# Kernel tuning notes

Hardware: AMD Instinct MI355X
Metric: run time of the kernel (lower is better)

Reference implementation:

```python
import jax, jax.numpy as jnp
import numpy as np

N, C, K, B, G = 32768, 128, 16, 4, 8
SCALE, BASE = 2.0, 10000.0

def _bn(x, gamma, beta, eps=1e-5):
    # torch BatchNorm1d (training): stats over all axes except channel (last)
    axes = tuple(range(x.ndim - 1))
    mean = x.mean(axes)
    var = x.var(axes)
    return (x - mean) / jnp.sqrt(var + eps) * gamma + beta

def _cayley_rope(x, coord, S_param):
    c = x.shape[-1]
    S = jnp.triu(S_param, 1)
    S = S - S.T
    I = jnp.eye(c, dtype=x.dtype)
    P = jnp.linalg.solve(I + S, I - S)  # (I+S)^-1 (I-S)
    xr = x @ P.T
    dpa = c // 3 // 2 * 2          # dim per axis (even)
    dr = dpa * 3                   # rotated dims
    inv_freq = 1.0 / (BASE ** (jnp.arange(0, dpa, 2, dtype=jnp.float32) / dpa))
    cs = coord * SCALE
    def rot(f, c1):
        ang = c1[:, None] * inv_freq[None, :]
        s, co = jnp.sin(ang), jnp.cos(ang)
        fr, fi = jnp.split(f, 2, axis=-1)
        return jnp.concatenate([fr * co - fi * s, fr * s + fi * co], -1)
    parts = [rot(xr[:, i * dpa:(i + 1) * dpa], cs[:, i]) for i in range(3)]
    out = jnp.concatenate(parts + [xr[:, dr:]], -1)
    return out @ P

def setup_inputs() -> dict:
    key = jax.random.key(0)
    ks = jax.random.split(key, 24)
    w = lambda k, i, o, s=0.02: jax.random.normal(k, (i, o), jnp.float32) * s
    inp = {
        'feat': jax.random.normal(ks[0], (N, C), jnp.float32),
        'coord': jax.random.uniform(ks[1], (N, 3), jnp.float32) * 10.0,
        'reference_index': jax.random.randint(ks[2], (N, K), 0, N),
        'offset': jnp.arange(1, B + 1, dtype=jnp.int32) * (N // B),
        'Wq': w(ks[3], C, C), 'bq': jnp.zeros((C,)),
        'gq': jnp.ones((C,)), 'bnq': jnp.zeros((C,)),
        'Wk': w(ks[4], C, C), 'bk': jnp.zeros((C,)),
        'gk': jnp.ones((C,)), 'bnk': jnp.zeros((C,)),
        'Wv': w(ks[5], C, C), 'bv': jnp.zeros((C,)),
        'S_param': jax.random.normal(ks[6], (C, C), jnp.float32) * 0.01,
        'Ww1': w(ks[7], C, G), 'bw1': jnp.zeros((G,)),
        'gw': jnp.ones((G,)), 'bnw': jnp.zeros((G,)),
        'Ww2': w(ks[8], G, G), 'bw2': jnp.zeros((G,)),
        'Wg1': w(ks[9], 2 * C, C), 'bg1': jnp.zeros((C,)),
        'gg': jnp.ones((C,)), 'bng': jnp.zeros((C,)),
        'Wg2': w(ks[10], C, G, 0.001), 'bg2': jnp.full((G,), 3.0),
    }
    return inp

def reference(feat, coord, reference_index, offset, Wq, bq, gq, bnq, Wk, bk, gk, bnk,
              Wv, bv, S_param, Ww1, bw1, gw, bnw, Ww2, bw2, Wg1, bg1, gg, bng, Wg2, bg2):
    q_raw = jax.nn.relu(_bn(feat @ Wq + bq, gq, bnq))
    k_raw = jax.nn.relu(_bn(feat @ Wk + bk, gk, bnk))
    value = feat @ Wv + bv
    q = _cayley_rope(q_raw, coord, S_param)
    k = _cayley_rope(k_raw, coord, S_param)
    kg = k[reference_index]            # [N,K,C] gather
    vg = value[reference_index]        # [N,K,C]
    rel = kg - q[:, None, :]
    geom = jax.nn.relu(_bn(rel @ Ww1 + bw1, gw, bnw)) @ Ww2 + bw2  # [N,K,G]
    seg = jnp.searchsorted(offset, jnp.arange(N), side='right')
    gmax = jax.ops.segment_max(q_raw, seg, num_segments=B)
    gate_in = jnp.concatenate([q_raw, gmax[seg]], -1)              # [N,2C]
    gate = jax.nn.sigmoid(jax.nn.relu(_bn(gate_in @ Wg1 + bg1, gg, bng)) @ Wg2 + bg2)  # [N,G]
    refined = geom * (1.0 + gate[:, None, :])
    attn = jax.nn.softmax(refined, axis=1)
    mask = jnp.sign(reference_index + 1).astype(attn.dtype)
    attn = attn * mask[:, :, None]
    vg4 = vg.reshape(N, K, G, C // G)
    out = jnp.einsum('nkgi,nkg->ngi', vg4, attn).reshape(N, C)
    return out
```

## Files before the change

### kernel.cpp

```cpp
#include <hip/hip_runtime.h>
#include <math.h>

#define N_PTS 32768
#define C_DIM 128
#define K_NB  16
#define G_DIM 8

#define OF_PW     0
#define OF_STATQ  1024
#define OF_STATK  1280
#define OF_STATG1 1536
#define OF_STATH  1792
#define OF_UMAXP  1808
#define OF_UMAXN  2320
#define OF_WQT    4096
#define OF_WKT    12288
#define OF_WVT    20480
#define OF_WG1T   28672
#define OF_PTMIT  36864
#define OF_QW     65536
#define OF_KW     327680
#define OF_GATE   589824
#define OF_G1     1048576
#define OF_V      5242880

typedef short bf16x8 __attribute__((ext_vector_type(8)));
typedef float f32x4  __attribute__((ext_vector_type(4)));

#define LSTR 136

__device__ __forceinline__ unsigned f2bf(float f) {
  unsigned u = __float_as_uint(f);
  return (u + 0x7fffu + ((u >> 16) & 1u)) >> 16;
}
__device__ __forceinline__ float bf2f(short s) {
  return __uint_as_float(((unsigned)(unsigned short)s) << 16);
}
__device__ __forceinline__ unsigned fenc(float f) {
  unsigned b = __float_as_uint(f);
  return (b & 0x80000000u) ? ~b : (b | 0x80000000u);
}
__device__ __forceinline__ float fdec(unsigned u) {
  unsigned b = (u & 0x80000000u) ? (u & 0x7fffffffu) : ~u;
  return __uint_as_float(b);
}
__device__ __forceinline__ bf16x8 pack_bf8(float4 a, float4 b) {
  bf16x8 r;
  r[0] = (short)f2bf(a.x); r[1] = (short)f2bf(a.y);
  r[2] = (short)f2bf(a.z); r[3] = (short)f2bf(a.w);
  r[4] = (short)f2bf(b.x); r[5] = (short)f2bf(b.y);
  r[6] = (short)f2bf(b.z); r[7] = (short)f2bf(b.w);
  return r;
}
__device__ __forceinline__ float fetch_asym(const float* M, int r, int c) {
  return (c > r) ? M[r*128 + c] : ((c < r) ? -M[c*128 + r] : 0.f);
}

__device__ __forceinline__ void g2l16(const void* g, void* l) {
  __builtin_amdgcn_global_load_lds(
      (const __attribute__((address_space(1))) void*)g,
      (__attribute__((address_space(3))) void*)l, 16, 0, 0);
}

__device__ __forceinline__ void stage_async(short* dst, const short* __restrict__ src, int tid) {
  int lane = tid & 63, wv = tid >> 6;
  #pragma unroll
  for (int it = 0; it < 8; ++it) {
    int chunk = it*256 + wv*64;
    int D = (chunk + lane)*16;
    int gs = D ^ (((D >> 8) & 7) << 4);
    g2l16((const char*)src + gs, (char*)dst + chunk*16);
  }
}

__device__ __forceinline__ f32x4 mfma1(const short* Bb, const bf16x8* a4, int row, int quad) {
  f32x4 ac = {0.f, 0.f, 0.f, 0.f};
  int sx = (row & 7) << 4;
  #pragma unroll
  for (int ks = 0; ks < 4; ++ks) {
    const char* p = (const char*)Bb + (((row*256) + ks*64 + quad*16) ^ sx);
    ac = __builtin_amdgcn_mfma_f32_16x16x32_bf16(a4[ks], *(const bf16x8*)p, ac, 0, 0, 0);
  }
  return ac;
}

__global__ __launch_bounds__(256) void cayley(const float* __restrict__ Sp,
    const float* __restrict__ Ww1,
    const float* __restrict__ Wq, const float* __restrict__ Wk,
    const float* __restrict__ Wv, const float* __restrict__ Wg1,
    short* __restrict__ WqT, short* __restrict__ WkT,
    short* __restrict__ WvT, short* __restrict__ Wg1T,
    short* __restrict__ PTmIT, float* __restrict__ PW,
    float* __restrict__ statz)
{
  __shared__ short Ssh[128*LSTR];
  __shared__ float x0[128], x1[128];
  int bx = blockIdx.x, tid = threadIdx.x;
  if (bx >= 64) {
    if (bx < 80) {
      int idx = bx - 64, widx = idx >> 2, qr = idx & 3;
      const float* src = (widx == 0) ? Wq : (widx == 1) ? Wk : (widx == 2) ? Wv : Wg1;
      short* dst = (widx == 0) ? WqT : (widx == 1) ? WkT : (widx == 2) ? WvT : Wg1T;
      const float4* s4 = (const float4*)src;
      #pragma unroll
      for (int it = 0; it < 4; ++it) {
        int q = it*256 + tid; int k = qr*32 + (q >> 5), n4 = q & 31;
        float4 v = s4[k*32 + n4];
        dst[(n4*4+0)*128 + k] = (short)f2bf(v.x);
        dst[(n4*4+1)*128 + k] = (short)f2bf(v.y);
        dst[(n4*4+2)*128 + k] = (short)f2bf(v.z);
        dst[(n4*4+3)*128 + k] = (short)f2bf(v.w);
      }
    } else {
      #pragma unroll
      for (int it = 0; it < 8; ++it) {
        int idx = it*256 + tid;
        if (idx < 1808) statz[idx] = 0.f;
      }
    }
    return;
  }
  int c0 = bx*2, c1 = c0 + 1;
  #pragma unroll 8
  for (int it = 0; it < 64; ++it) {
    int idx = it*256 + tid; int i = idx >> 7, j = idx & 127;
    Ssh[i*LSTR + j] = (short)f2bf(fetch_asym(Sp, i, j));
  }
  if (tid < 128) {
    x0[tid] = (tid == c0) ? 1.f : 0.f;
    x1[tid] = (tid == c1) ? 1.f : 0.f;
  }
  __syncthreads();
  int i = tid >> 1, h = tid & 1;
  const short* srow = &Ssh[i*LSTR + h*64];
  for (int t = 0; t < 16; ++t) {
    float a0 = 0.f, a1 = 0.f;
    #pragma unroll
    for (int jq = 0; jq < 16; ++jq) {
      short4 sv = *(const short4*)&srow[jq*4];
      #pragma unroll
      for (int u = 0; u < 4; ++u) {
        float s = bf2f((&sv.x)[u]);
        int j = h*64 + jq*4 + u;
        a0 = fmaf(s, x0[j], a0);
        a1 = fmaf(s, x1[j], a1);
      }
    }
    a0 += __shfl_xor(a0, 1);
    a1 += __shfl_xor(a1, 1);
    __syncthreads();
    if (h == 0) {
      x0[i] = a0 + ((i == c0) ? 1.f : 0.f);
      x1[i] = a1 + ((i == c1) ? 1.f : 0.f);
    }
    __syncthreads();
  }
  if (tid < 128) {
    PTmIT[c0*128 + tid] = (short)f2bf(2.f*x0[tid] - ((tid == c0) ? 2.f : 0.f));
  } else {
    int t = tid - 128;
    PTmIT[c1*128 + t] = (short)f2bf(2.f*x1[t] - ((t == c1) ? 2.f : 0.f));
  }
  if (tid < 16) {
    int cc = tid >> 3, g = tid & 7;
    const float* xv = cc ? x1 : x0;
    int c = cc ? c1 : c0;
    float acc = 0.f;
    #pragma unroll 8
    for (int j = 0; j < 128; ++j) acc = fmaf(xv[j], Ww1[j*8 + g], acc);
    PW[c*8 + g] = 2.f*acc - Ww1[c*8 + g];
  }
}

__global__ __launch_bounds__(256, 2) void qkv_mfma(const float* __restrict__ feat,
    const short* __restrict__ WqT, const short* __restrict__ WkT, const short* __restrict__ WvT,
    const float* __restrict__ bq, const float* __restrict__ bk, const float* __restrict__ bv,
    float* __restrict__ Vv,
    float* __restrict__ statq, float* __restrict__ statk,
    unsigned* __restrict__ umaxp, unsigned* __restrict__ umaxn)
{
  __shared__ __align__(16) short Bb0[128*128];
  __shared__ __align__(16) short Bb1[128*128];
  __shared__ float ssum[2][128], ssq[2][128];
  __shared__ unsigned ump[128], umn[128];
  int tid = threadIdx.x, row0 = blockIdx.x * 64, seg = row0 >> 13;
  int lane = tid & 63, w = tid >> 6, l15 = lane & 15, quad = lane >> 4;
  stage_async(Bb0, WqT, tid);
  if (tid < 128) {
    ssum[0][tid] = 0.f; ssum[1][tid] = 0.f;
    ssq[0][tid] = 0.f;  ssq[1][tid] = 0.f;
    ump[tid] = 0u; umn[tid] = 0u;
  }
  bf16x8 af[4];
  {
    long rbase = (long)(row0 + w*16 + l15) * 128;
    #pragma unroll
    for (int ks = 0; ks < 4; ++ks) {
      int c0 = ks*32 + quad*8;
      float4 v0 = *(const float4*)&feat[rbase + c0];
      float4 v1 = *(const float4*)&feat[rbase + c0 + 4];
      af[ks] = pack_bf8(v0, v1);
    }
  }
  __syncthreads();
  stage_async(Bb1, WkT, tid);
  {
    #pragma unroll
    for (int nt = 0; nt < 8; ++nt) {
      f32x4 ac = mfma1(Bb0, af, nt*16 + l15, quad);
      int col = nt*16 + l15;
      float bb = bq[col];
      float s = 0.f, s2 = 0.f, mx = -1e30f, mn = 1e30f;
      #pragma unroll
      for (int r = 0; r < 4; ++r) {
        float raw = ac[r];
        float v = raw + bb;
        s += v; s2 = fmaf(v, v, s2);
        mx = fmaxf(mx, raw); mn = fminf(mn, raw);
      }
      s += __shfl_xor(s, 16); s += __shfl_xor(s, 32);
      s2 += __shfl_xor(s2, 16); s2 += __shfl_xor(s2, 32);
      mx = fmaxf(mx, __shfl_xor(mx, 16)); mx = fmaxf(mx, __shfl_xor(mx, 32));
      mn = fminf(mn, __shfl_xor(mn, 16)); mn = fminf(mn, __shfl_xor(mn, 32));
      if (lane < 16) {
        atomicAdd(&ssum[0][col], s); atomicAdd(&ssq[0][col], s2);
        atomicMax(&ump[col], fenc(mx)); atomicMax(&umn[col], fenc(-mn));
      }
    }
  }
  __syncthreads();
  stage_async(Bb0, WvT, tid);
  {
    #pragma unroll
    for (int nt = 0; nt < 8; ++nt) {
      f32x4 ac = mfma1(Bb1, af, nt*16 + l15, quad);
      int col = nt*16 + l15;
      float bb = bk[col];
      float s = 0.f, s2 = 0.f;
      #pragma unroll
      for (int r = 0; r < 4; ++r) {
        float v = ac[r] + bb;
        s += v; s2 = fmaf(v, v, s2);
      }
      s += __shfl_xor(s, 16); s += __shfl_xor(s, 32);
      s2 += __shfl_xor(s2, 16); s2 += __shfl_xor(s2, 32);
      if (lane < 16) { atomicAdd(&ssum[1][col], s); atomicAdd(&ssq[1][col], s2); }
    }
  }
  __syncthreads();
  {
    #pragma unroll
    for (int nt = 0; nt < 8; ++nt) {
      f32x4 ac = mfma1(Bb0, af, nt*16 + l15, quad);
      int col = nt*16 + l15;
      float bb = bv[col];
      #pragma unroll
      for (int r = 0; r < 4; ++r)
        Vv[(long)(row0 + w*16 + quad*4 + r)*128 + col] = ac[r] + bb;
    }
  }
  __syncthreads();
  if (tid < 128) {
    atomicAdd(&statq[tid], ssum[0][tid]); atomicAdd(&statq[128 + tid], ssq[0][tid]);
    atomicAdd(&statk[tid], ssum[1][tid]); atomicAdd(&statk[128 + tid], ssq[1][tid]);
    atomicMax(&umaxp[seg*128 + tid], ump[tid]);
    atomicMax(&umaxn[seg*128 + tid], umn[tid]);
  }
}

__global__ __launch_bounds__(256) void rqkw(
    const float* __restrict__ feat,
    const short* __restrict__ WqT, const short* __restrict__ WkT,
    const short* __restrict__ PTmIT, const short* __restrict__ Wg1T,
    const float* __restrict__ coord,
    const float* __restrict__ bq, const float* __restrict__ bk,
    const float* __restrict__ statq, const float* __restrict__ statk,
    const float* __restrict__ gq, const float* __restrict__ bnq,
    const float* __restrict__ gk, const float* __restrict__ bnk,
    const unsigned* __restrict__ umaxp, const unsigned* __restrict__ umaxn,
    const float* __restrict__ Wg1, const float* __restrict__ bg1,
    const float* __restrict__ PW, const float* __restrict__ bw1,
    float* __restrict__ qw, float* __restrict__ kw,
    float* __restrict__ g1, float* __restrict__ statg1)
{
  __shared__ __align__(16) char arena[58880];
  __shared__ float caq[128], cbq[128], cak[128], cbk[128];
  __shared__ float gml[128], gsg[128];
  __shared__ float ssum[128], ssq[128];
  short* featS = (short*)arena;
  short* bnqS  = (short*)(arena + 8704);
  short* bnkS  = (short*)(arena + 17408);
  short* Bbuf  = (short*)(arena + 26112);
  float* xsq = (float*)arena;
  float* xsk = (float*)(arena + 16896);
  float* pws = (float*)(arena + 33792);
  int tid = threadIdx.x;
  int row0 = blockIdx.x * 32, seg = row0 >> 13;
  const float invn = 1.f / 32768.f;
  stage_async(Bbuf, WqT, tid);
  if (tid < 128) {
    float m = statq[tid]*invn, vv = fmaf(-m, m, statq[128 + tid]*invn);
    float a = rsqrtf(vv + 1e-5f) * gq[tid];
    float b = fmaf(-m, a, bnq[tid]);
    float cb2 = fmaf(a, bq[tid], b);
    caq[tid] = a; cbq[tid] = cb2;
    float mx = fdec(umaxp[seg*128 + tid]);
    float mn = -fdec(umaxn[seg*128 + tid]);
    gml[tid] = fmaxf(0.f, fmaxf(fmaf(a, mx, cb2), fmaf(a, mn, cb2)));
    m = statk[tid]*invn; vv = fmaf(-m, m, statk[128 + tid]*invn);
    a = rsqrtf(vv + 1e-5f) * gk[tid];
    b = fmaf(-m, a, bnk[tid]);
    cak[tid] = a; cbk[tid] = fmaf(a, bk[tid], b);
    ssum[tid] = 0.f; ssq[tid] = 0.f;
  }
  {
    const float4* s4 = (const float4*)feat;
    #pragma unroll
    for (int it = 0; it < 4; ++it) {
      int q = it*256 + tid; int r = q >> 5, c4 = q & 31;
      float4 v = s4[(long)(row0 + r)*32 + c4];
      uint2 p;
      p.x = f2bf(v.x) | (f2bf(v.y) << 16);
      p.y = f2bf(v.z) | (f2bf(v.w) << 16);
      *(uint2*)&featS[r*LSTR + c4*4] = p;
    }
  }
  __syncthreads();
  int lane = tid & 63, w = tid >> 6, l15 = lane & 15, quad = lane >> 4;
  bool isq = (w < 2);
  int rw = (w & 1) * 16;
  const float* ca = isq ? caq : cak;
  const float* cb = isq ? cbq : cbk;
  bf16x8 af[4];
  #pragma unroll
  for (int ks = 0; ks < 4; ++ks)
    af[ks] = *(bf16x8*)&featS[(rw + l15)*LSTR + ks*32 + quad*8];

  float bnl[32];
  if (isq) {
    #pragma unroll
    for (int nt = 0; nt < 8; ++nt) {
      f32x4 ac = mfma1(Bbuf, af, nt*16 + l15, quad);
      int col = nt*16 + l15;
      float A = ca[col], B = cb[col];
      #pragma unroll
      for (int r = 0; r < 4; ++r) {
        float v = fmaxf(0.f, fmaf(A, ac[r], B));
        bnl[nt*4 + r] = v;
        bnqS[(rw + quad*4 + r)*LSTR + col] = (short)f2bf(v);
      }
    }
  }
  __syncthreads();
  stage_async(Bbuf, WkT, tid);
  __syncthreads();
  if (!isq) {
    #pragma unroll
    for (int nt = 0; nt < 8; ++nt) {
      f32x4 ac = mfma1(Bbuf, af, nt*16 + l15, quad);
      int col = nt*16 + l15;
      float A = ca[col], B = cb[col];
      #pragma unroll
      for (int r = 0; r < 4; ++r) {
        float v = fmaxf(0.f, fmaf(A, ac[r], B));
        bnl[nt*4 + r] = v;
        bnkS[(rw + quad*4 + r)*LSTR + col] = (short)f2bf(v);
      }
    }
  } else if (tid < 128) {
    float acc = bg1[tid];
    #pragma unroll 8
    for (int j = 0; j < 128; ++j)
      acc = fmaf(gml[j], Wg1[(128 + j)*128 + tid], acc);
    gsg[tid] = acc;
  }
  __syncthreads();
  stage_async(Bbuf, PTmIT, tid);
  bf16x8 af2[4];
  {
    const short* bnS = isq ? bnqS : bnkS;
    #pragma unroll
    for (int ks = 0; ks < 4; ++ks)
      af2[ks] = *(bf16x8*)&bnS[(rw + l15)*LSTR + ks*32 + quad*8];
  }
  __syncthreads();
  f32x4 accv[8];
  #pragma unroll
  for (int nt = 0; nt < 8; ++nt)
    accv[nt] = mfma1(Bbuf, af2, nt*16 + l15, quad);
  __syncthreads();
  stage_async(Bbuf, Wg1T, tid);
  __syncthreads();
  f32x4 accw[8];
  if (isq) {
    #pragma unroll
    for (int nt = 0; nt < 8; ++nt)
      accw[nt] = mfma1(Bbuf, af2, nt*16 + l15, quad);
  }
  __syncthreads();
  {
    float* xs = isq ? xsq : xsk;
    #pragma unroll
    for (int nt = 0; nt < 8; ++nt) {
      int col = nt*16 + l15;
      #pragma unroll
      for (int r = 0; r < 4; ++r)
        xs[(rw + quad*4 + r)*132 + col] = accv[nt][r] + bnl[nt*4 + r];
    }
  }
  #pragma unroll
  for (int it = 0; it < 4; ++it) { int idx = tid + it*256; pws[idx] = PW[idx]; }
  if (isq) {
    #pragma unroll
    for (int nt = 0; nt < 8; ++nt) {
      int col = nt*16 + l15;
      float gsv = gsg[col];
      float s = 0.f, s2 = 0.f;
      #pragma unroll
      for (int r = 0; r < 4; ++r) {
        float v = accw[nt][r] + gsv;
        int row = row0 + rw + quad*4 + r;
        g1[(long)row*128 + col] = v;
        s += v; s2 = fmaf(v, v, s2);
      }
      s += __shfl_xor(s, 16); s += __shfl_xor(s, 32);
      s2 += __shfl_xor(s2, 16); s2 += __shfl_xor(s2, 32);
      if (lane < 16) { atomicAdd(&ssum[col], s); atomicAdd(&ssq[col], s2); }
    }
  }
  __syncthreads();
  #pragma unroll
  for (int it = 0; it < 8; ++it) {
    int idx = it*256 + tid;
    int r = idx >> 6, s = idx & 63;
    if (s < 63) {
      int a3 = s / 21, j = s - a3*21;
      int cr = a3*42 + j;
      float invf = exp2f((float)(2*j) * (-13.287712379549449f / 42.f));
      float ang = coord[(row0 + r)*3 + a3] * (2.0f * invf);
      float sn, co; sincosf(ang, &sn, &co);
      float fr = xsq[r*132 + cr], fi = xsq[r*132 + cr + 21];
      xsq[r*132 + cr]      = fr*co - fi*sn;
      xsq[r*132 + cr + 21] = fr*sn + fi*co;
      fr = xsk[r*132 + cr]; fi = xsk[r*132 + cr + 21];
      xsk[r*132 + cr]      = fr*co - fi*sn;
      xsk[r*132 + cr + 21] = fr*sn + fi*co;
    }
  }
  __syncthreads();
  #pragma unroll
  for (int it = 0; it < 2; ++it) {
    int idx = it*256 + tid;
    int mat = idx >> 8, r2 = (idx >> 3) & 31, g = idx & 7;
    const float* x2 = mat ? xsk : xsq;
    float a0 = 0.f, a1 = 0.f, a2 = 0.f, a3 = 0.f;
    #pragma unroll 8
    for (int i = 0; i < 128; i += 4) {
      float4 xv = *(const float4*)&x2[r2*132 + i];
      a0 = fmaf(xv.x, pws[(i+0)*8 + g], a0);
      a1 = fmaf(xv.y, pws[(i+1)*8 + g], a1);
      a2 = fmaf(xv.z, pws[(i+2)*8 + g], a2);
      a3 = fmaf(xv.w, pws[(i+3)*8 + g], a3);
    }
    float acc = (a0 + a1) + (a2 + a3) + (mat ? bw1[g] : 0.f);
    float* dst = mat ? kw : qw;
    dst[(long)(row0 + r2)*8 + g] = acc;
  }
  if (tid < 128) {
    atomicAdd(&statg1[tid], ssum[tid]);
    atomicAdd(&statg1[128 + tid], ssq[tid]);
  }
}

__global__ __launch_bounds__(256) void mid(
    const float* __restrict__ g1, const float* __restrict__ statg1,
    const float* __restrict__ ggm, const float* __restrict__ bng,
    const float* __restrict__ Wg2, const float* __restrict__ bg2,
    float* __restrict__ gate,
    const float* __restrict__ kw, const float* __restrict__ qw,
    const int* __restrict__ ref, float* __restrict__ stath)
{
  __shared__ float gs[32][132];
  __shared__ float w2s[128][8];
  __shared__ float cA[128], cB[128];
  __shared__ float red[256];
  int tid = threadIdx.x;
  if (blockIdx.x < 1024) {
    int row0 = blockIdx.x * 32;
    #pragma unroll
    for (int it = 0; it < 4; ++it) { int idx = tid + it*256; w2s[idx >> 3][idx & 7] = Wg2[idx]; }
    if (tid < 128) {
      const float invn = 1.f / 32768.f;
      float m = statg1[tid]*invn, v = fmaf(-m, m, statg1[128 + tid]*invn);
      float a = rsqrtf(v + 1e-5f) * ggm[tid];
      cA[tid] = a; cB[tid] = fmaf(-m, a, bng[tid]);
    }
    #pragma unroll
    for (int it = 0; it < 4; ++it) {
      int idx = tid + it*256; int r = idx >> 5, cq = idx & 31;
      *(float4*)&gs[r][cq*4] = *(const float4*)&g1[(long)(row0 + r)*128 + cq*4];
    }
    __syncthreads();
    int r = tid >> 3, g = tid & 7;
    float acc = bg2[g];
    #pragma unroll 8
    for (int c2 = 0; c2 < 128; ++c2) {
      float act = fmaxf(0.f, fmaf(gs[r][c2], cA[c2], cB[c2]));
      acc = fmaf(act, w2s[c2][g], acc);
    }
    gate[(long)(row0 + r)*8 + g] = 1.f / (1.f + expf(-acc));
  } else {
    long base = (long)(blockIdx.x - 1024) * 4096;
    float s = 0.f, sq = 0.f;
    for (int it = 0; it < 16; ++it) {
      long idx = base + it*256 + tid;
      int n = (int)(idx >> 7); int kk = (int)((idx >> 3) & 15); int g = (int)(idx & 7);
      int r = ref[n*16 + kk];
      float h = kw[(long)r*8 + g] - qw[(long)n*8 + g];
      s += h; sq = fmaf(h, h, sq);
    }
    red[tid] = s; __syncthreads();
    for (int d = 128; d >= 8; d >>= 1) { if (tid < d) red[tid] += red[tid + d]; __syncthreads(); }
    if (tid < 8) atomicAdd(&stath[tid], red[tid]);
    __syncthreads();
    red[tid] = sq; __syncthreads();
    for (int d = 128; d >= 8; d >>= 1) { if (tid < d) red[tid] += red[tid + d]; __syncthreads(); }
    if (tid < 8) atomicAdd(&stath[8 + tid], red[tid]);
  }
}

__global__ __launch_bounds__(256) void attn_out(const float* __restrict__ qw, const float* __restrict__ kw,
                                                const float* __restrict__ stath,
                                                const float* __restrict__ gw, const float* __restrict__ bnw,
                                                const float* __restrict__ Ww2, const float* __restrict__ bw2,
                                                const float* __restrict__ gate, const int* __restrict__ ref,
                                                const float* __restrict__ v, float* __restrict__ out)
{
  __shared__ float sm1[2][16][9];
  __shared__ float sm2[2][16][9];
  __shared__ int   smr[2][16];
  int tid = threadIdx.x; int rh = tid >> 7, t = tid & 127;
  int n = blockIdx.x * 2 + rh;
  int kk = t >> 3, g = t & 7;
  if (t < 16) smr[rh][t] = ref[n*16 + t];
  __syncthreads();
  const float invnk = 1.f / 524288.f;
  float m0 = stath[g]*invnk, v0 = fmaf(-m0, m0, stath[8 + g]*invnk);
  float aw = rsqrtf(v0 + 1e-5f) * gw[g];
  float bw = fmaf(-m0, aw, bnw[g]);
  int rr = smr[rh][kk];
  float h = kw[(long)rr*8 + g] - qw[(long)n*8 + g];
  sm1[rh][kk][g] = fmaxf(0.f, fmaf(h, aw, bw));
  __syncthreads();
  float acc = bw2[g];
  #pragma unroll
  for (int g2 = 0; g2 < 8; ++g2) acc = fmaf(sm1[rh][kk][g2], Ww2[g2*8 + g], acc);
  float refined = acc * (1.f + gate[(long)n*8 + g]);
  sm2[rh][kk][g] = refined;
  __syncthreads();
  float mx = -1e30f;
  #pragma unroll
  for (int k2 = 0; k2 < 16; ++k2) mx = fmaxf(mx, sm2[rh][k2][g]);
  float e = expf(refined - mx);
  sm1[rh][kk][g] = e;
  __syncthreads();
  float ssum = 0.f;
  #pragma unroll
  for (int k2 = 0; k2 < 16; ++k2) ssum += sm1[rh][k2][g];
  float mask = ((rr + 1) > 0) ? 1.f : (((rr + 1) == 0) ? 0.f : -1.f);
  float attn = e / ssum * mask;
  sm2[rh][kk][g] = attn;
  __syncthreads();
  float o = 0.f;
  #pragma unroll
  for (int k2 = 0; k2 < 16; ++k2) {
    o = fmaf(v[(long)smr[rh][k2]*128 + t], sm2[rh][k2][t >> 4], o);
  }
  out[(long)n*128 + t] = o;
}

extern "C" void kernel_launch(void* const* d_in, const int* in_sizes, int n_in,
                              void* d_out, int out_size, void* d_ws, size_t ws_size,
                              hipStream_t stream)
{
  const float* feat  = (const float*)d_in[0];
  const float* coord = (const float*)d_in[1];
  const int*   ref   = (const int*)d_in[2];
  const float* Wq  = (const float*)d_in[4];
  const float* bq  = (const float*)d_in[5];
  const float* gq  = (const float*)d_in[6];
  const float* bnq = (const float*)d_in[7];
  const float* Wk  = (const float*)d_in[8];
  const float* bk  = (const float*)d_in[9];
  const float* gk  = (const float*)d_in[10];
  const float* bnk = (const float*)d_in[11];
  const float* Wv  = (const float*)d_in[12];
  const float* bv  = (const float*)d_in[13];
  const float* Sp  = (const float*)d_in[14];
  const float* Ww1 = (const float*)d_in[15];
  const float* bw1 = (const float*)d_in[16];
  const float* gw  = (const float*)d_in[17];
  const float* bnw = (const float*)d_in[18];
  const float* Ww2 = (const float*)d_in[19];
  const float* bw2 = (const float*)d_in[20];
  const float* Wg1 = (const float*)d_in[21];
  const float* bg1 = (const float*)d_in[22];
  const float* ggm = (const float*)d_in[23];
  const float* bng = (const float*)d_in[24];
  const float* Wg2 = (const float*)d_in[25];
  const float* bg2 = (const float*)d_in[26];
  float* out = (float*)d_out;

  float* W = (float*)d_ws;
  float* PW = W + OF_PW;
  short* WqT   = (short*)(W + OF_WQT);
  short* WkT   = (short*)(W + OF_WKT);
  short* WvT   = (short*)(W + OF_WVT);
  short* Wg1T  = (short*)(W + OF_WG1T);
  short* PTmIT = (short*)(W + OF_PTMIT);
  float* G1 = W + OF_G1;
  float* Vv = W + OF_V;

  cayley<<<81, 256, 0, stream>>>(Sp, Ww1, Wq, Wk, Wv, Wg1,
                                 WqT, WkT, WvT, Wg1T, PTmIT, PW, W + OF_STATQ);
  qkv_mfma<<<512, 256, 0, stream>>>(feat, WqT, WkT, WvT, bq, bk, bv, Vv,
                                    W + OF_STATQ, W + OF_STATK,
                                    (unsigned*)(W + OF_UMAXP), (unsigned*)(W + OF_UMAXN));
  rqkw<<<1024, 256, 0, stream>>>(feat, WqT, WkT, PTmIT, Wg1T, coord,
                                 bq, bk,
                                 W + OF_STATQ, W + OF_STATK,
                                 gq, bnq, gk, bnk,
                                 (const unsigned*)(W + OF_UMAXP), (const unsigned*)(W + OF_UMAXN),
                                 Wg1, bg1, PW, bw1,
                                 W + OF_QW, W + OF_KW, G1, W + OF_STATG1);
  mid<<<2048, 256, 0, stream>>>(G1, W + OF_STATG1, ggm, bng, Wg2, bg2, W + OF_GATE,
                                W + OF_KW, W + OF_QW, ref, W + OF_STATH);
  attn_out<<<16384, 256, 0, stream>>>(W + OF_QW, W + OF_KW, W + OF_STATH, gw, bnw, Ww2, bw2,
                                      W + OF_GATE, ref, Vv, out);
}
```

Before: 316.9 us.

## Split rqkw into separate q and k blocks to cut LDS and raise occupancy

```diff
diff --git a/kernel.cpp b/kernel.cpp
--- a/kernel.cpp
+++ b/kernel.cpp
@@ -268,7 +268,7 @@
   }
 }
 
-__global__ __launch_bounds__(256) void rqkw(
+__global__ __launch_bounds__(256, 3) void rqkw(
     const float* __restrict__ feat,
     const short* __restrict__ WqT, const short* __restrict__ WkT,
     const short* __restrict__ PTmIT, const short* __restrict__ Wg1T,
@@ -283,150 +283,116 @@
     float* __restrict__ qw, float* __restrict__ kw,
     float* __restrict__ g1, float* __restrict__ statg1)
 {
-  __shared__ __align__(16) char arena[58880];
-  __shared__ float caq[128], cbq[128], cak[128], cbk[128];
-  __shared__ float gml[128], gsg[128];
-  __shared__ float ssum[128], ssq[128];
-  short* featS = (short*)arena;
-  short* bnqS  = (short*)(arena + 8704);
-  short* bnkS  = (short*)(arena + 17408);
-  short* Bbuf  = (short*)(arena + 26112);
-  float* xsq = (float*)arena;
-  float* xsk = (float*)(arena + 16896);
-  float* pws = (float*)(arena + 33792);
-  int tid = threadIdx.x;
-  int row0 = blockIdx.x * 32, seg = row0 >> 13;
+  __shared__ __align__(16) char arena[41472];
+  __shared__ float ca[128], cb[128];
+  __shared__ float gml[128], gsg[128], ssum[128], ssq[128];
+  short* Bbuf = (short*)arena;
+  short* bnS  = (short*)(arena + 32768);
+  float* xs   = (float*)arena;
+  float* pws  = (float*)(arena + 16896);
+  int tid = threadIdx.x, bx = blockIdx.x;
+  bool isq = (bx & 1) == 0;
+  int row0 = (bx >> 1) * 32, seg = row0 >> 13;
+  int lane = tid & 63, w = tid >> 6, l15 = lane & 15, quad = lane >> 4;
+  int mrow = (w & 1) * 16;
+  int nt0  = (w >> 1) * 4;
+  stage_async(Bbuf, isq ? WqT : WkT, tid);
+  bf16x8 af[4];
+  {
+    long rbase = (long)(row0 + mrow + l15) * 128;
+    #pragma unroll
+    for (int ks = 0; ks < 4; ++ks) {
+      int c0 = ks*32 + quad*8;
+      float4 v0 = *(const float4*)&feat[rbase + c0];
+      float4 v1 = *(const float4*)&feat[rbase + c0 + 4];
+      af[ks] = pack_bf8(v0, v1);
+    }
+  }
   const float invn = 1.f / 32768.f;
-  stage_async(Bbuf, WqT, tid);
   if (tid < 128) {
-    float m = statq[tid]*invn, vv = fmaf(-m, m, statq[128 + tid]*invn);
-    float a = rsqrtf(vv + 1e-5f) * gq[tid];
-    float b = fmaf(-m, a, bnq[tid]);
-    float cb2 = fmaf(a, bq[tid], b);
-    caq[tid] = a; cbq[tid] = cb2;
-    float mx = fdec(umaxp[seg*128 + tid]);
-    float mn = -fdec(umaxn[seg*128 + tid]);
-    gml[tid] = fmaxf(0.f, fmaxf(fmaf(a, mx, cb2), fmaf(a, mn, cb2)));
-    m = statk[tid]*invn; vv = fmaf(-m, m, statk[128 + tid]*invn);
-    a = rsqrtf(vv + 1e-5f) * gk[tid];
-    b = fmaf(-m, a, bnk[tid]);
-    cak[tid] = a; cbk[tid] = fmaf(a, bk[tid], b);
-    ssum[tid] = 0.f; ssq[tid] = 0.f;
-  }
-  {
-    const float4* s4 = (const float4*)feat;
-    #pragma unroll
-    for (int it = 0; it < 4; ++it) {
-      int q = it*256 + tid; int r = q >> 5, c4 = q & 31;
-      float4 v = s4[(long)(row0 + r)*32 + c4];
-      uint2 p;
-      p.x = f2bf(v.x) | (f2bf(v.y) << 16);
-      p.y = f2bf(v.z) | (f2bf(v.w) << 16);
-      *(uint2*)&featS[r*LSTR + c4*4] = p;
-    }
-  }
-  __syncthreads();
-  int lane = tid & 63, w = tid >> 6, l15 = lane & 15, quad = lane >> 4;
-  bool isq = (w < 2);
-  int rw = (w & 1) * 16;
-  const float* ca = isq ? caq : cak;
-  const float* cb = isq ? cbq : cbk;
-  bf16x8 af[4];
-  #pragma unroll
-  for (int ks = 0; ks < 4; ++ks)
-    af[ks] = *(bf16x8*)&featS[(rw + l15)*LSTR + ks*32 + quad*8];
-
-  float bnl[32];
-  if (isq) {
-    #pragma unroll
-    for (int nt = 0; nt < 8; ++nt) {
-      f32x4 ac = mfma1(Bbuf, af, nt*16 + l15, quad);
-      int col = nt*16 + l15;
-      float A = ca[col], B = cb[col];
-      #pragma unroll
-      for (int r = 0; r < 4; ++r) {
-        float v = fmaxf(0.f, fmaf(A, ac[r], B));
-        bnl[nt*4 + r] = v;
-        bnqS[(rw + quad*4 + r)*LSTR + col] = (short)f2bf(v);
-      }
-    }
-  }
-  __syncthreads();
-  stage_async(Bbuf, WkT, tid);
-  __syncthreads();
-  if (!isq) {
-    #pragma unroll
-    for (int nt = 0; nt < 8; ++nt) {
-      f32x4 ac = mfma1(Bbuf, af, nt*16 + l15, quad);
-      int col = nt*16 + l15;
-      float A = ca[col], B = cb[col];
-      #pragma unroll
-      for (int r = 0; r < 4; ++r) {
-        float v = fmaxf(0.f, fmaf(A, ac[r], B));
-        bnl[nt*4 + r] = v;
-        bnkS[(rw + quad*4 + r)*LSTR + col] = (short)f2bf(v);
-      }
-    }
-  } else if (tid < 128) {
+    if (isq) {
+      float m = statq[tid]*invn, vv = fmaf(-m, m, statq[128 + tid]*invn);
+      float a = rsqrtf(vv + 1e-5f) * gq[tid];
+      float b = fmaf(-m, a, bnq[tid]);
+      float cb2 = fmaf(a, bq[tid], b);
+      ca[tid] = a; cb[tid] = cb2;
+      float mx = fdec(umaxp[seg*128 + tid]);
+      float mn = -fdec(umaxn[seg*128 + tid]);
+      gml[tid] = fmaxf(0.f, fmaxf(fmaf(a, mx, cb2), fmaf(a, mn, cb2)));
+      ssum[tid] = 0.f; ssq[tid] = 0.f;
+    } else {
+      float m = statk[tid]*invn, vv = fmaf(-m, m, statk[128 + tid]*invn);
+      float a = rsqrtf(vv + 1e-5f) * gk[tid];
+      float b = fmaf(-m, a, bnk[tid]);
+      ca[tid] = a; cb[tid] = fmaf(a, bk[tid], b);
+    }
+  }
+  __syncthreads();
+  float bnl[16];
+  #pragma unroll
+  for (int nt = 0; nt < 4; ++nt) {
+    f32x4 ac = mfma1(Bbuf, af, (nt0 + nt)*16 + l15, quad);
+    int col = (nt0 + nt)*16 + l15;
+    float A = ca[col], B = cb[col];
+    #pragma unroll
+    for (int r = 0; r < 4; ++r) {
+      float v = fmaxf(0.f, fmaf(A, ac[r], B));
+      bnl[nt*4 + r] = v;
+      bnS[(mrow + quad*4 + r)*LSTR + col] = (short)f2bf(v);
+    }
+  }
+  __syncthreads();
+  stage_async(Bbuf, PTmIT, tid);
+  if (isq && tid < 128) {
     float acc = bg1[tid];
     #pragma unroll 8
     for (int j = 0; j < 128; ++j)
       acc = fmaf(gml[j], Wg1[(128 + j)*128 + tid], acc);
     gsg[tid] = acc;
   }
-  __syncthreads();
-  stage_async(Bbuf, PTmIT, tid);
   bf16x8 af2[4];
-  {
-    const short* bnS = isq ? bnqS : bnkS;
-    #pragma unroll
-    for (int ks = 0; ks < 4; ++ks)
-      af2[ks] = *(bf16x8*)&bnS[(rw + l15)*LSTR + ks*32 + quad*8];
-  }
-  __syncthreads();
-  f32x4 accv[8];
-  #pragma unroll
-  for (int nt = 0; nt < 8; ++nt)
-    accv[nt] = mfma1(Bbuf, af2, nt*16 + l15, quad);
-  __syncthreads();
-  stage_async(Bbuf, Wg1T, tid);
-  __syncthreads();
-  f32x4 accw[8];
+  #pragma unroll
+  for (int ks = 0; ks < 4; ++ks)
+    af2[ks] = *(bf16x8*)&bnS[(mrow + l15)*LSTR + ks*32 + quad*8];
+  __syncthreads();
+  f32x4 accv[4];
+  #pragma unroll
+  for (int nt = 0; nt < 4; ++nt)
+    accv[nt] = mfma1(Bbuf, af2, (nt0 + nt)*16 + l15, quad);
+  __syncthreads();
   if (isq) {
-    #pragma unroll
-    for (int nt = 0; nt < 8; ++nt)
-      accw[nt] = mfma1(Bbuf, af2, nt*16 + l15, quad);
-  }
-  __syncthreads();
-  {
-    float* xs = isq ? xsq : xsk;
-    #pragma unroll
-    for (int nt = 0; nt < 8; ++nt) {
-      int col = nt*16 + l15;
-      #pragma unroll
-      for (int r = 0; r < 4; ++r)
-        xs[(rw + quad*4 + r)*132 + col] = accv[nt][r] + bnl[nt*4 + r];
-    }
-  }
-  #pragma unroll
-  for (int it = 0; it < 4; ++it) { int idx = tid + it*256; pws[idx] = PW[idx]; }
-  if (isq) {
-    #pragma unroll
-    for (int nt = 0; nt < 8; ++nt) {
-      int col = nt*16 + l15;
+    stage_async(Bbuf, Wg1T, tid);
+    __syncthreads();
+    #pragma unroll
+    for (int nt = 0; nt < 4; ++nt) {
+      f32x4 ac = mfma1(Bbuf, af2, (nt0 + nt)*16 + l15, quad);
+      int col = (nt0 + nt)*16 + l15;
       float gsv = gsg[col];
       float s = 0.f, s2 = 0.f;
       #pragma unroll
       for (int r = 0; r < 4; ++r) {
-        float v = accw[nt][r] + gsv;
-        int row = row0 + rw + quad*4 + r;
-        g1[(long)row*128 + col] = v;
+        float v = ac[r] + gsv;
+        g1[(long)(row0 + mrow + quad*4 + r)*128 + col] = v;
         s += v; s2 = fmaf(v, v, s2);
       }
       s += __shfl_xor(s, 16); s += __shfl_xor(s, 32);
       s2 += __shfl_xor(s2, 16); s2 += __shfl_xor(s2, 32);
       if (lane < 16) { atomicAdd(&ssum[col], s); atomicAdd(&ssq[col], s2); }
     }
+    __syncthreads();
+  }
+  #pragma unroll
+  for (int nt = 0; nt < 4; ++nt) {
+    int col = (nt0 + nt)*16 + l15;
+    #pragma unroll
+    for (int r = 0; r < 4; ++r)
+      xs[(mrow + quad*4 + r)*132 + col] = accv[nt][r] + bnl[nt*4 + r];
+  }
+  #pragma unroll
+  for (int it = 0; it < 4; ++it) { int idx = tid + it*256; pws[idx] = PW[idx]; }
+  if (isq && tid < 128) {
+    atomicAdd(&statg1[tid], ssum[tid]);
+    atomicAdd(&statg1[128 + tid], ssq[tid]);
   }
   __syncthreads();
   #pragma unroll
@@ -439,36 +405,26 @@
       float invf = exp2f((float)(2*j) * (-13.287712379549449f / 42.f));
       float ang = coord[(row0 + r)*3 + a3] * (2.0f * invf);
       float sn, co; sincosf(ang, &sn, &co);
-      float fr = xsq[r*132 + cr], fi = xsq[r*132 + cr + 21];
-      xsq[r*132 + cr]      = fr*co - fi*sn;
-      xsq[r*132 + cr + 21] = fr*sn + fi*co;
-      fr = xsk[r*132 + cr]; fi = xsk[r*132 + cr + 21];
-      xsk[r*132 + cr]      = fr*co - fi*sn;
-      xsk[r*132 + cr + 21] = fr*sn + fi*co;
-    }
-  }
-  __syncthreads();
-  #pragma unroll
-  for (int it = 0; it < 2; ++it) {
-    int idx = it*256 + tid;
-    int mat = idx >> 8, r2 = (idx >> 3) & 31, g = idx & 7;
-    const float* x2 = mat ? xsk : xsq;
+      float fr = xs[r*132 + cr], fi = xs[r*132 + cr + 21];
+      xs[r*132 + cr]      = fr*co - fi*sn;
+      xs[r*132 + cr + 21] = fr*sn + fi*co;
+    }
+  }
+  __syncthreads();
+  {
+    int r2 = tid >> 3, g = tid & 7;
     float a0 = 0.f, a1 = 0.f, a2 = 0.f, a3 = 0.f;
     #pragma unroll 8
     for (int i = 0; i < 128; i += 4) {
-      float4 xv = *(const float4*)&x2[r2*132 + i];
+      float4 xv = *(const float4*)&xs[r2*132 + i];
       a0 = fmaf(xv.x, pws[(i+0)*8 + g], a0);
       a1 = fmaf(xv.y, pws[(i+1)*8 + g], a1);
       a2 = fmaf(xv.z, pws[(i+2)*8 + g], a2);
       a3 = fmaf(xv.w, pws[(i+3)*8 + g], a3);
     }
-    float acc = (a0 + a1) + (a2 + a3) + (mat ? bw1[g] : 0.f);
-    float* dst = mat ? kw : qw;
+    float acc = (a0 + a1) + (a2 + a3) + (isq ? 0.f : bw1[g]);
+    float* dst = isq ? qw : kw;
     dst[(long)(row0 + r2)*8 + g] = acc;
-  }
-  if (tid < 128) {
-    atomicAdd(&statg1[tid], ssum[tid]);
-    atomicAdd(&statg1[128 + tid], ssq[tid]);
   }
 }
 
@@ -626,7 +582,7 @@
   qkv_mfma<<<512, 256, 0, stream>>>(feat, WqT, WkT, WvT, bq, bk, bv, Vv,
                                     W + OF_STATQ, W + OF_STATK,
                                     (unsigned*)(W + OF_UMAXP), (unsigned*)(W + OF_UMAXN));
-  rqkw<<<1024, 256, 0, stream>>>(feat, WqT, WkT, PTmIT, Wg1T, coord,
+  rqkw<<<2048, 256, 0, stream>>>(feat, WqT, WkT, PTmIT, Wg1T, coord,
                                  bq, bk,
                                  W + OF_STATQ, W + OF_STATK,
                                  gq, bnq, gk, bnk,
```

After: 321.9 us. No clear change (+1.6%).

## Double-buffer weight staging in rqkw and hoist gate-max projection into a prep kernel

Applied to the files above, without the earlier changes.

```diff
diff --git a/kernel.cpp b/kernel.cpp
--- a/kernel.cpp
+++ b/kernel.cpp
@@ -13,6 +13,7 @@
 #define OF_STATH  1792
 #define OF_UMAXP  1808
 #define OF_UMAXN  2320
+#define OF_GSG    2832
 #define OF_WQT    4096
 #define OF_WKT    12288
 #define OF_WVT    20480
@@ -268,7 +269,35 @@
   }
 }
 
-__global__ __launch_bounds__(256) void rqkw(
+__global__ __launch_bounds__(128) void gprep(
+    const float* __restrict__ statq,
+    const float* __restrict__ gq, const float* __restrict__ bnq,
+    const float* __restrict__ bq,
+    const unsigned* __restrict__ umaxp, const unsigned* __restrict__ umaxn,
+    const float* __restrict__ Wg1, const float* __restrict__ bg1,
+    float* __restrict__ gsgO)
+{
+  __shared__ float gml[128];
+  int s = blockIdx.x, tid = threadIdx.x;
+  const float invn = 1.f / 32768.f;
+  {
+    float m = statq[tid]*invn, vv = fmaf(-m, m, statq[128 + tid]*invn);
+    float a = rsqrtf(vv + 1e-5f) * gq[tid];
+    float b = fmaf(-m, a, bnq[tid]);
+    float cb2 = fmaf(a, bq[tid], b);
+    float mx = fdec(umaxp[s*128 + tid]);
+    float mn = -fdec(umaxn[s*128 + tid]);
+    gml[tid] = fmaxf(0.f, fmaxf(fmaf(a, mx, cb2), fmaf(a, mn, cb2)));
+  }
+  __syncthreads();
+  float acc = bg1[tid];
+  #pragma unroll 8
+  for (int j = 0; j < 128; ++j)
+    acc = fmaf(gml[j], Wg1[(128 + j)*128 + tid], acc);
+  gsgO[s*128 + tid] = acc;
+}
+
+__global__ __launch_bounds__(256, 2) void rqkw(
     const float* __restrict__ feat,
     const short* __restrict__ WqT, const short* __restrict__ WkT,
     const short* __restrict__ PTmIT, const short* __restrict__ Wg1T,
@@ -277,156 +306,150 @@
     const float* __restrict__ statq, const float* __restrict__ statk,
     const float* __restrict__ gq, const float* __restrict__ bnq,
     const float* __restrict__ gk, const float* __restrict__ bnk,
-    const unsigned* __restrict__ umaxp, const unsigned* __restrict__ umaxn,
-    const float* __restrict__ Wg1, const float* __restrict__ bg1,
+    const float* __restrict__ gsgG,
     const float* __restrict__ PW, const float* __restrict__ bw1,
     float* __restrict__ qw, float* __restrict__ kw,
     float* __restrict__ g1, float* __restrict__ statg1)
 {
-  __shared__ __align__(16) char arena[58880];
-  __shared__ float caq[128], cbq[128], cak[128], cbk[128];
-  __shared__ float gml[128], gsg[128];
-  __shared__ float ssum[128], ssq[128];
-  short* featS = (short*)arena;
-  short* bnqS  = (short*)(arena + 8704);
-  short* bnkS  = (short*)(arena + 17408);
-  short* Bbuf  = (short*)(arena + 26112);
-  float* xsq = (float*)arena;
-  float* xsk = (float*)(arena + 16896);
-  float* pws = (float*)(arena + 33792);
-  int tid = threadIdx.x;
-  int row0 = blockIdx.x * 32, seg = row0 >> 13;
-  const float invn = 1.f / 32768.f;
-  stage_async(Bbuf, WqT, tid);
-  if (tid < 128) {
-    float m = statq[tid]*invn, vv = fmaf(-m, m, statq[128 + tid]*invn);
-    float a = rsqrtf(vv + 1e-5f) * gq[tid];
-    float b = fmaf(-m, a, bnq[tid]);
-    float cb2 = fmaf(a, bq[tid], b);
-    caq[tid] = a; cbq[tid] = cb2;
-    float mx = fdec(umaxp[seg*128 + tid]);
-    float mn = -fdec(umaxn[seg*128 + tid]);
-    gml[tid] = fmaxf(0.f, fmaxf(fmaf(a, mx, cb2), fmaf(a, mn, cb2)));
-    m = statk[tid]*invn; vv = fmaf(-m, m, statk[128 + tid]*invn);
-    a = rsqrtf(vv + 1e-5f) * gk[tid];
-    b = fmaf(-m, a, bnk[tid]);
-    cak[tid] = a; cbk[tid] = fmaf(a, bk[tid], b);
-    ssum[tid] = 0.f; ssq[tid] = 0.f;
-  }
-  {
-    const float4* s4 = (const float4*)feat;
-    #pragma unroll
-    for (int it = 0; it < 4; ++it) {
-      int q = it*256 + tid; int r = q >> 5, c4 = q & 31;
-      float4 v = s4[(long)(row0 + r)*32 + c4];
-      uint2 p;
-      p.x = f2bf(v.x) | (f2bf(v.y) << 16);
-      p.y = f2bf(v.z) | (f2bf(v.w) << 16);
-      *(uint2*)&featS[r*LSTR + c4*4] = p;
-    }
-  }
-  __syncthreads();
+  __shared__ __align__(16) char arena[81920];
+  short* Bb0  = (short*)arena;
+  short* Bb1  = (short*)(arena + 32768);
+  char*  bnqS = arena + 65536;
+  char*  bnkS = arena + 73728;
+  float* ssum = (float*)(arena + 65536);
+  float* ssq  = (float*)(arena + 66048);
+  float* xsq  = (float*)arena;
+  float* xsk  = (float*)(arena + 16896);
+  float* pws  = (float*)(arena + 33792);
+  int tid = threadIdx.x, row0 = blockIdx.x * 32, seg = row0 >> 13;
   int lane = tid & 63, w = tid >> 6, l15 = lane & 15, quad = lane >> 4;
   bool isq = (w < 2);
   int rw = (w & 1) * 16;
-  const float* ca = isq ? caq : cak;
-  const float* cb = isq ? cbq : cbk;
+  stage_async(Bb0, WqT, tid);
+  stage_async(Bb1, WkT, tid);
   bf16x8 af[4];
-  #pragma unroll
-  for (int ks = 0; ks < 4; ++ks)
-    af[ks] = *(bf16x8*)&featS[(rw + l15)*LSTR + ks*32 + quad*8];
-
+  {
+    long rbase = (long)(row0 + rw + l15) * 128;
+    #pragma unroll
+    for (int ks = 0; ks < 4; ++ks) {
+      int c0 = ks*32 + quad*8;
+      float4 v0 = *(const float4*)&feat[rbase + c0];
+      float4 v1 = *(const float4*)&feat[rbase + c0 + 4];
+      af[ks] = pack_bf8(v0, v1);
+    }
+  }
+  float caR[8], cbR[8];
+  {
+    const float* stat = isq ? statq : statk;
+    const float* gg   = isq ? gq : gk;
+    const float* bn_  = isq ? bnq : bnk;
+    const float* bb_  = isq ? bq : bk;
+    const float invn = 1.f / 32768.f;
+    #pragma unroll
+    for (int nt = 0; nt < 8; ++nt) {
+      int col = nt*16 + l15;
+      float m = stat[col]*invn, vv = fmaf(-m, m, stat[128 + col]*invn);
+      float a = rsqrtf(vv + 1e-5f) * gg[col];
+      float b = fmaf(-m, a, bn_[col]);
+      caR[nt] = a; cbR[nt] = fmaf(a, bb_[col], b);
+    }
+  }
+  __syncthreads();
   float bnl[32];
   if (isq) {
     #pragma unroll
     for (int nt = 0; nt < 8; ++nt) {
-      f32x4 ac = mfma1(Bbuf, af, nt*16 + l15, quad);
-      int col = nt*16 + l15;
-      float A = ca[col], B = cb[col];
+      f32x4 ac = mfma1(Bb0, af, nt*16 + l15, quad);
+      int col = nt*16 + l15;
+      float A = caR[nt], B = cbR[nt];
       #pragma unroll
       for (int r = 0; r < 4; ++r) {
         float v = fmaxf(0.f, fmaf(A, ac[r], B));
         bnl[nt*4 + r] = v;
-        bnqS[(rw + quad*4 + r)*LSTR + col] = (short)f2bf(v);
-      }
-    }
-  }
-  __syncthreads();
-  stage_async(Bbuf, WkT, tid);
-  __syncthreads();
+        int row = rw + quad*4 + r;
+        int ba = (row*256 + col*2) ^ ((row & 7) << 4);
+        *(short*)(bnqS + ba) = (short)f2bf(v);
+      }
+    }
+  }
+  __syncthreads();
+  stage_async(Bb0, PTmIT, tid);
   if (!isq) {
     #pragma unroll
     for (int nt = 0; nt < 8; ++nt) {
-      f32x4 ac = mfma1(Bbuf, af, nt*16 + l15, quad);
-      int col = nt*16 + l15;
-      float A = ca[col], B = cb[col];
+      f32x4 ac = mfma1(Bb1, af, nt*16 + l15, quad);
+      int col = nt*16 + l15;
+      float A = caR[nt], B = cbR[nt];
       #pragma unroll
       for (int r = 0; r < 4; ++r) {
         float v = fmaxf(0.f, fmaf(A, ac[r], B));
         bnl[nt*4 + r] = v;
-        bnkS[(rw + quad*4 + r)*LSTR + col] = (short)f2bf(v);
-      }
-    }
-  } else if (tid < 128) {
-    float acc = bg1[tid];
-    #pragma unroll 8
-    for (int j = 0; j < 128; ++j)
-      acc = fmaf(gml[j], Wg1[(128 + j)*128 + tid], acc);
-    gsg[tid] = acc;
-  }
-  __syncthreads();
-  stage_async(Bbuf, PTmIT, tid);
+        int row = rw + quad*4 + r;
+        int ba = (row*256 + col*2) ^ ((row & 7) << 4);
+        *(short*)(bnkS + ba) = (short)f2bf(v);
+      }
+    }
+  }
+  __syncthreads();
+  stage_async(Bb1, Wg1T, tid);
   bf16x8 af2[4];
   {
-    const short* bnS = isq ? bnqS : bnkS;
+    const char* bs = isq ? bnqS : bnkS;
+    int rowA = rw + l15, sx2 = (rowA & 7) << 4;
     #pragma unroll
     for (int ks = 0; ks < 4; ++ks)
-      af2[ks] = *(bf16x8*)&bnS[(rw + l15)*LSTR + ks*32 + quad*8];
-  }
-  __syncthreads();
+      af2[ks] = *(const bf16x8*)(bs + ((rowA*256 + ks*64 + quad*16) ^ sx2));
+  }
+  float gsR[8];
+  if (isq) {
+    #pragma unroll
+    for (int nt = 0; nt < 8; ++nt)
+      gsR[nt] = gsgG[seg*128 + nt*16 + l15];
+  }
   f32x4 accv[8];
   #pragma unroll
   for (int nt = 0; nt < 8; ++nt)
-    accv[nt] = mfma1(Bbuf, af2, nt*16 + l15, quad);
-  __syncthreads();
-  stage_async(Bbuf, Wg1T, tid);
-  __syncthreads();
-  f32x4 accw[8];
+    accv[nt] = mfma1(Bb0, af2, nt*16 + l15, quad);
+  __syncthreads();
+  if (tid >= 128) {
+    int c = tid - 128;
+    ssum[c] = 0.f; ssq[c] = 0.f;
+  }
+  __syncthreads();
   if (isq) {
     #pragma unroll
-    for (int nt = 0; nt < 8; ++nt)
-      accw[nt] = mfma1(Bbuf, af2, nt*16 + l15, quad);
-  }
-  __syncthreads();
-  {
-    float* xs = isq ? xsq : xsk;
-    #pragma unroll
-    for (int nt = 0; nt < 8; ++nt) {
-      int col = nt*16 + l15;
-      #pragma unroll
-      for (int r = 0; r < 4; ++r)
-        xs[(rw + quad*4 + r)*132 + col] = accv[nt][r] + bnl[nt*4 + r];
-    }
-  }
-  #pragma unroll
-  for (int it = 0; it < 4; ++it) { int idx = tid + it*256; pws[idx] = PW[idx]; }
-  if (isq) {
-    #pragma unroll
-    for (int nt = 0; nt < 8; ++nt) {
-      int col = nt*16 + l15;
-      float gsv = gsg[col];
+    for (int nt = 0; nt < 8; ++nt) {
+      f32x4 ac = mfma1(Bb1, af2, nt*16 + l15, quad);
+      int col = nt*16 + l15;
+      float gsv = gsR[nt];
       float s = 0.f, s2 = 0.f;
       #pragma unroll
       for (int r = 0; r < 4; ++r) {
-        float v = accw[nt][r] + gsv;
-        int row = row0 + rw + quad*4 + r;
-        g1[(long)row*128 + col] = v;
+        float v = ac[r] + gsv;
+        g1[(long)(row0 + rw + quad*4 + r)*128 + col] = v;
         s += v; s2 = fmaf(v, v, s2);
       }
       s += __shfl_xor(s, 16); s += __shfl_xor(s, 32);
       s2 += __shfl_xor(s2, 16); s2 += __shfl_xor(s2, 32);
       if (lane < 16) { atomicAdd(&ssum[col], s); atomicAdd(&ssq[col], s2); }
     }
+  }
+  __syncthreads();
+  {
+    float* xs = isq ? xsq : xsk;
+    #pragma unroll
+    for (int nt = 0; nt < 8; ++nt) {
+      int col = nt*16 + l15;
+      #pragma unroll
+      for (int r = 0; r < 4; ++r)
+        xs[(rw + quad*4 + r)*132 + col] = accv[nt][r] + bnl[nt*4 + r];
+    }
+  }
+  #pragma unroll
+  for (int it = 0; it < 4; ++it) { int idx = tid + it*256; pws[idx] = PW[idx]; }
+  if (tid < 128) {
+    atomicAdd(&statg1[tid], ssum[tid]);
+    atomicAdd(&statg1[128 + tid], ssq[tid]);
   }
   __syncthreads();
   #pragma unroll
@@ -465,10 +488,6 @@
     float acc = (a0 + a1) + (a2 + a3) + (mat ? bw1[g] : 0.f);
     float* dst = mat ? kw : qw;
     dst[(long)(row0 + r2)*8 + g] = acc;
-  }
-  if (tid < 128) {
-    atomicAdd(&statg1[tid], ssum[tid]);
-    atomicAdd(&statg1[128 + tid], ssq[tid]);
   }
 }
 
@@ -626,12 +645,15 @@
   qkv_mfma<<<512, 256, 0, stream>>>(feat, WqT, WkT, WvT, bq, bk, bv, Vv,
                                     W + OF_STATQ, W + OF_STATK,
                                     (unsigned*)(W + OF_UMAXP), (unsigned*)(W + OF_UMAXN));
+  gprep<<<4, 128, 0, stream>>>(W + OF_STATQ, gq, bnq, bq,
+                               (const unsigned*)(W + OF_UMAXP),
+                               (const unsigned*)(W + OF_UMAXN),
+                               Wg1, bg1, W + OF_GSG);
   rqkw<<<1024, 256, 0, stream>>>(feat, WqT, WkT, PTmIT, Wg1T, coord,
                                  bq, bk,
                                  W + OF_STATQ, W + OF_STATK,
                                  gq, bnq, gk, bnk,
-                                 (const unsigned*)(W + OF_UMAXP), (const unsigned*)(W + OF_UMAXN),
-                                 Wg1, bg1, PW, bw1,
+                                 W + OF_GSG, PW, bw1,
                                  W + OF_QW, W + OF_KW, G1, W + OF_STATG1);
   mid<<<2048, 256, 0, stream>>>(G1, W + OF_STATG1, ggm, bng, Wg2, bg2, W + OF_GATE,
                                 W + OF_KW, W + OF_QW, ref, W + OF_STATH);
```

Result: no change. 318.8 us (+0.6%).
